# Optimization experiments

Hardware: AMD Instinct MI355X
Metric: run time of the kernel (lower is better)

## Reference

```python
import jax, jax.numpy as jnp
import numpy as np

N, S, D = 8, 448, 768
VS, DS = 50000, 256
VP, DP = 200, 128
VM, DM = 400, 128
VA, DA = 360, 128
EPS_LS = 0.1
LN_EPS = 1e-12
SQRT2 = 1.4142135623730951


def setup_inputs() -> dict:
    key = jax.random.key(0)
    ks = jax.random.split(key, 20)
    total = N * S
    # all sequence lengths == S; next-token prediction uses tokens [0, S-2] as
    # inputs (hidden_sel) and tokens [1, S-1] as targets (target_sel)
    hidden_sel = np.concatenate([i * S + np.arange(S - 1) for i in range(N)]).astype(np.int32)
    target_sel = np.concatenate([i * S + np.arange(1, S) for i in range(N)]).astype(np.int32)
    tokens_lengths = (np.arange(total) % 4).astype(np.int32)  # per-token affix counts
    affix_sel = np.nonzero(tokens_lengths[target_sel] > 0)[0].astype(np.int32)

    def p(k, shape):
        return jax.random.normal(k, shape, jnp.float32) * 0.02

    inp = {
        "tr_hidden_state": jax.random.normal(ks[0], (S, N, D), jnp.float32),
        "affixes_prob": jax.random.uniform(ks[1], (total, VA), dtype=jnp.float32),
        "stems": jax.random.randint(ks[2], (total,), 0, VS, jnp.int32),
        "pos_tags": jax.random.randint(ks[3], (total,), 0, VP, jnp.int32),
        "lm_morphs": jax.random.randint(ks[4], (total,), 0, VM, jnp.int32),
        "hidden_sel_idx": jnp.asarray(hidden_sel),
        "target_sel_idx": jnp.asarray(target_sel),
        "affix_sel_idx": jnp.asarray(affix_sel),
        # stem head
        "stem_emb": p(ks[5], (VS, DS)), "stem_W": p(ks[6], (D, DS)),
        "stem_b": jnp.zeros((DS,)), "stem_g": jnp.ones((DS,)),
        "stem_beta": jnp.zeros((DS,)), "stem_bias": jnp.zeros((VS,)),
        # pos-tag head
        "pos_emb": p(ks[7], (VP, DP)), "pos_W": p(ks[8], (D, DP)),
        "pos_b": jnp.zeros((DP,)), "pos_g": jnp.ones((DP,)),
        "pos_beta": jnp.zeros((DP,)), "pos_bias": jnp.zeros((VP,)),
        # lm-morph head
        "morph_emb": p(ks[9], (VM, DM)), "morph_W": p(ks[10], (D, DM)),
        "morph_b": jnp.zeros((DM,)), "morph_g": jnp.ones((DM,)),
        "morph_beta": jnp.zeros((DM,)), "morph_bias": jnp.zeros((VM,)),
        # affixes head
        "aff_emb": p(ks[11], (VA, DA)), "aff_W": p(ks[12], (D, DA)),
        "aff_b": jnp.zeros((DA,)), "aff_g": jnp.ones((DA,)),
        "aff_beta": jnp.zeros((DA,)), "aff_bias": jnp.zeros((VA,)),
    }
    return inp


def _gelu(x):
    return x * 0.5 * (1.0 + jax.lax.erf(x / SQRT2))


def _ln(x, g, b):
    m = x.mean(-1, keepdims=True)
    v = ((x - m) ** 2).mean(-1, keepdims=True)
    return (x - m) * jax.lax.rsqrt(v + LN_EPS) * g + b


def _head(x, W, b, g, beta, emb, bias):
    h = _ln(_gelu(x @ W + b), g, beta)  # BaseHeadTransform
    return h @ emb.T + bias             # tied decoder + bias


def _ls_nll(lprobs, tgt):
    # label_smoothed_nll_loss with reduce=True, no ignore_index
    nll = -jnp.take_along_axis(lprobs, tgt[:, None], axis=1)[:, 0]
    smooth = -lprobs.sum(-1)
    nll_m, sm_m = nll.mean(), smooth.mean()
    eps_i = EPS_LS / (lprobs.shape[-1] - 1)
    return (1.0 - EPS_LS - eps_i) * nll_m + eps_i * sm_m, nll_m


def reference(tr_hidden_state, affixes_prob, stems, pos_tags, lm_morphs,
              hidden_sel_idx, target_sel_idx, affix_sel_idx,
              stem_emb, stem_W, stem_b, stem_g, stem_beta, stem_bias,
              pos_emb, pos_W, pos_b, pos_g, pos_beta, pos_bias,
              morph_emb, morph_W, morph_b, morph_g, morph_beta, morph_bias,
              aff_emb, aff_W, aff_b, aff_g, aff_beta, aff_bias):
    flat = jnp.transpose(tr_hidden_state, (1, 0, 2)).reshape(N * S, D)
    x = flat[hidden_sel_idx]  # [T, D] ragged gather of predictor states

    stem_lp = jax.nn.log_softmax(_head(x, stem_W, stem_b, stem_g, stem_beta, stem_emb, stem_bias), axis=-1)
    stem_loss, stem_nll = _ls_nll(stem_lp, stems[target_sel_idx])

    pos_lp = jax.nn.log_softmax(_head(x, pos_W, pos_b, pos_g, pos_beta, pos_emb, pos_bias), axis=-1)
    pos_loss, pos_nll = _ls_nll(pos_lp, pos_tags[target_sel_idx])

    morph_lp = jax.nn.log_softmax(_head(x, morph_W, morph_b, morph_g, morph_beta, morph_emb, morph_bias), axis=-1)
    morph_loss, morph_nll = _ls_nll(morph_lp, lm_morphs[target_sel_idx])

    xa = x[affix_sel_idx]                                # tokens with affixes
    ta = affixes_prob[target_sel_idx][affix_sel_idx]     # [Ta, VA]
    z = _head(xa, aff_W, aff_b, aff_g, aff_beta, aff_emb, aff_bias)
    aff_loss = jnp.mean(jnp.maximum(z, 0.0) - z * ta + jnp.log1p(jnp.exp(-jnp.abs(z))))

    return jnp.stack([stem_loss, pos_loss, morph_loss, aff_loss, stem_nll, pos_nll, morph_nll])
```

## Files before the change

kernel.cpp:

```cpp
#include <hip/hip_runtime.h>
#include <cstdint>
#include <cstddef>


typedef __attribute__((ext_vector_type(8))) __bf16 bf16x8;
typedef __attribute__((ext_vector_type(4))) float f32x4;
typedef __attribute__((ext_vector_type(4))) unsigned short u16x4;
typedef __attribute__((ext_vector_type(2))) unsigned short u16x2;

namespace {
constexpr int S_LEN   = 448;
constexpr int N_SEQ   = 8;
constexpr int D_MODEL = 768;
constexpr int TPAD    = 3584;
constexpr int VS = 50000, VP = 200, VM = 400, VA = 360;
constexpr int DS_STEM = 256, DS_POS = 128, DS_MORPH = 128, DS_AFF = 128;
constexpr int VS_PAD = 50176;
constexpr int VCHUNK = 32;
constexpr int VITERS = 3136 / VCHUNK;
constexpr int PERIODS = VITERS / 2;
constexpr float PAD_E = (float)(VS_PAD - VS);
constexpr int NVB_P = 1;
constexpr int NVB_M = 2;
constexpr float LOG2E = 1.4426950408889634f;
constexpr float LN2   = 0.6931471805599453f;
constexpr int B_STEM = 448;
constexpr int B_P    = B_STEM + 112;
constexpr int B_M    = B_P + 224;
constexpr int PREP_G = TPAD * D_MODEL / 256;
constexpr int PREP_T = PREP_G + 120;
constexpr int PREP_C = PREP_T + 12753;
}

__device__ __forceinline__ unsigned short f2bf(float f) {
  unsigned int u = __float_as_uint(f);
  unsigned int r = (u + 0x7FFFu + ((u >> 16) & 1u)) >> 16;
  return (unsigned short)r;
}
__device__ __forceinline__ float bf2f(unsigned short u) {
  return __uint_as_float(((unsigned int)u) << 16);
}
__device__ __forceinline__ float fexp2(float x) {
#if __has_builtin(__builtin_amdgcn_exp2f)
  return __builtin_amdgcn_exp2f(x);
#else
  return exp2f(x);
#endif
}

__global__ __launch_bounds__(256) void prep_kernel(
    const float* __restrict__ tr, const int* __restrict__ hsel,
    const int* __restrict__ tsel, const int* __restrict__ asel,
    const int* __restrict__ stems, const int* __restrict__ postags,
    const int* __restrict__ morphs,
    unsigned short* __restrict__ x, int* __restrict__ tgtS, int* __restrict__ tgtP,
    int* __restrict__ tgtM, int* __restrict__ arow, int T, int Ta,
    const float* __restrict__ sW, const float* __restrict__ pW,
    const float* __restrict__ mW, const float* __restrict__ aW,
    unsigned short* __restrict__ wtS, unsigned short* __restrict__ wtP,
    unsigned short* __restrict__ wtM, unsigned short* __restrict__ wtA,
    const float* __restrict__ sE, const float* __restrict__ pE,
    const float* __restrict__ mE, const float* __restrict__ aE,
    const float* __restrict__ sb,
    unsigned short* __restrict__ dS, unsigned short* __restrict__ dP,
    unsigned short* __restrict__ dM, unsigned short* __restrict__ dA,
    float* __restrict__ bp) {
  __shared__ float tile[64][65];
  const int bid = blockIdx.x;
  const int tid = threadIdx.x;
  if (bid < PREP_G) {
    const size_t e = (size_t)bid * 256 + tid;
    const int t = (int)(e / D_MODEL);
    const int d = (int)(e % D_MODEL);
    float v = 0.f;
    if (t < T) {
      int idx = hsel[t];
      int n = idx / S_LEN, s = idx % S_LEN;
      v = tr[((size_t)s * N_SEQ + n) * D_MODEL + d];
    }
    x[e] = f2bf(v);
    if (e < (size_t)T) {
      int tt = tsel[e];
      tgtS[e] = stems[tt]; tgtP[e] = postags[tt]; tgtM[e] = morphs[tt];
    }
    if (e < (size_t)Ta) arow[e] = tsel[asel[e]];
  } else if (bid < PREP_T) {
    const int tt = bid - PREP_G;
    const float* W; unsigned short* Wt; int DS, kt, nt;
    if (tt < 48) { W = sW; Wt = wtS; DS = 256; kt = tt >> 2; nt = tt & 3; }
    else {
      int u = tt - 48; const int h = u / 24; u %= 24;
      kt = u >> 1; nt = u & 1; DS = 128;
      W  = (h == 0) ? pW : (h == 1) ? mW : aW;
      Wt = (h == 0) ? wtP : (h == 1) ? wtM : wtA;
    }
    const int k0 = kt * 64, n0 = nt * 64;
    const int rr = tid >> 6, cc = tid & 63;
#pragma unroll
    for (int i = 0; i < 16; ++i)
      tile[i * 4 + rr][cc] = W[(size_t)(k0 + i * 4 + rr) * DS + n0 + cc];
    __syncthreads();
#pragma unroll
    for (int i = 0; i < 16; ++i)
      Wt[(size_t)(n0 + i * 4 + rr) * D_MODEL + k0 + cc] = f2bf(tile[cc][i * 4 + rr]);
  } else {
    const size_t q = ((size_t)(bid - PREP_T) * 256 + tid) * 4;
    if (q >= 13008896) {
      const size_t local = q - 13008896;
      float4 v = make_float4(0.f, 0.f, 0.f, 0.f);
      if (local < (size_t)VS) v = *(const float4*)(sb + local);
      v.x *= LOG2E; v.y *= LOG2E; v.z *= LOG2E; v.w *= LOG2E;
      *(float4*)(bp + local) = v;
      return;
    }
    const float* src; unsigned short* dst; size_t local, real;
    float sc = 1.f;
    if (q < 12845056)      { src = sE; dst = dS; local = q;            real = 12800000; sc = LOG2E; }
    else if (q < 12877824) { src = pE; dst = dP; local = q - 12845056; real = 25600; }
    else if (q < 12943360) { src = mE; dst = dM; local = q - 12877824; real = 51200; }
    else                   { src = aE; dst = dA; local = q - 12943360; real = 46080; }
    float4 v = make_float4(0.f, 0.f, 0.f, 0.f);
    if (local < real) v = *(const float4*)(src + local);
    u16x4 o = { f2bf(v.x * sc), f2bf(v.y * sc), f2bf(v.z * sc), f2bf(v.w * sc) };
    *(u16x4*)(dst + local) = o;
  }
}

template <int NT>
__device__ __forceinline__ void head_body(
    const unsigned short* __restrict__ x, const unsigned short* __restrict__ Wt,
    const float* __restrict__ bvec, const float* __restrict__ gvec,
    const float* __restrict__ betav, unsigned short* __restrict__ hout) {
  constexpr int DS = NT * 16;
  const int lane = threadIdx.x & 63;
  const int wave = threadIdx.x >> 6;
  const int row0 = blockIdx.x * 64 + wave * 16;
  const int lrow = lane & 15;
  const int lk8  = (lane >> 4) * 8;

  f32x4 acc[NT];
#pragma unroll
  for (int nt = 0; nt < NT; ++nt) acc[nt] = f32x4{0.f, 0.f, 0.f, 0.f};

  const unsigned short* xrow = x + (size_t)(row0 + lrow) * D_MODEL + lk8;
#pragma unroll
  for (int ks = 0; ks < 24; ++ks) {
    bf16x8 a = *(const bf16x8*)(xrow + ks * 32);
#pragma unroll
    for (int nt = 0; nt < NT; ++nt) {
      bf16x8 b = *(const bf16x8*)(Wt + (size_t)(nt * 16 + lrow) * D_MODEL + ks * 32 + lk8);
      acc[nt] = __builtin_amdgcn_mfma_f32_16x16x32_bf16(a, b, acc[nt], 0, 0, 0);
    }
  }

  float bb[NT], gg[NT], be[NT];
#pragma unroll
  for (int nt = 0; nt < NT; ++nt) {
    int c = nt * 16 + lrow;
    bb[nt] = bvec[c]; gg[nt] = gvec[c]; be[nt] = betav[c];
  }
#pragma unroll
  for (int r = 0; r < 4; ++r) {
    const int row = row0 + (lane >> 4) * 4 + r;
    float vals[NT];
    float s = 0.f, s2 = 0.f;
#pragma unroll
    for (int nt = 0; nt < NT; ++nt) {
      float v = acc[nt][r] + bb[nt];
      v = 0.5f * v * (1.f + erff(v * 0.70710678118654752f));
      vals[nt] = v; s += v; s2 += v * v;
    }
    s  += __shfl_xor(s, 1);  s  += __shfl_xor(s, 2);  s  += __shfl_xor(s, 4);  s  += __shfl_xor(s, 8);
    s2 += __shfl_xor(s2, 1); s2 += __shfl_xor(s2, 2); s2 += __shfl_xor(s2, 4); s2 += __shfl_xor(s2, 8);
    const float mean = s * (1.f / DS);
    const float var  = s2 * (1.f / DS) - mean * mean;
    const float rstd = rsqrtf(var + 1e-12f);
#pragma unroll
    for (int nt = 0; nt < NT; ++nt) {
      float o = (vals[nt] - mean) * rstd * gg[nt] + be[nt];
      hout[(size_t)row * DS + nt * 16 + lrow] = f2bf(o);
    }
  }
}

__global__ __launch_bounds__(256, 2) void head_all_kernel(
    const unsigned short* __restrict__ x,
    const unsigned short* __restrict__ wtS, const float* __restrict__ sb,
    const float* __restrict__ sg, const float* __restrict__ sbe, unsigned short* __restrict__ hS,
    const unsigned short* __restrict__ wtP, const float* __restrict__ pb,
    const float* __restrict__ pg, const float* __restrict__ pbe, unsigned short* __restrict__ hP,
    const unsigned short* __restrict__ wtM, const float* __restrict__ mb,
    const float* __restrict__ mg, const float* __restrict__ mbe, unsigned short* __restrict__ hM,
    const unsigned short* __restrict__ wtA, const float* __restrict__ ab,
    const float* __restrict__ ag, const float* __restrict__ abe, unsigned short* __restrict__ hA) {
  if (blockIdx.y == 3)      head_body<16>(x, wtS, sb, sg, sbe, hS);
  else if (blockIdx.y == 0) head_body<8>(x, wtP, pb, pg, pbe, hP);
  else if (blockIdx.y == 1) head_body<8>(x, wtM, mb, mg, mbe, hM);
  else                      head_body<8>(x, wtA, ab, ag, abe, hA);
}


__device__ __forceinline__ void stem_role(
    const unsigned short* __restrict__ h, const unsigned short* __restrict__ emb,
    const float* __restrict__ bpad, float* __restrict__ psum,
    float* __restrict__ psum2, char* smem) {
  float* lbias = (float*)(smem + 49152);

  const int f    = blockIdx.x;
  const int xcd  = f & 7;
  const int m    = f >> 3;
  const int bx   = m % 14;
  const int by   = (m / 14) * 8 + xcd;
  const int tid  = threadIdx.x;
  const int lane = tid & 63;
  const int wave = tid >> 6;
  const int lrow = lane & 15;
  const int hi   = lane >> 4;
  const int lk8  = hi * 8;
  const int tok0 = bx * 256 + wave * 64;
  const int vbase0 = by * (VITERS * 16);

  for (int i = tid; i < VITERS * 16; i += 256) lbias[i] = bpad[vbase0 + i];

  bf16x8 hB[4][8];
#pragma unroll
  for (int tt = 0; tt < 4; ++tt)
#pragma unroll
    for (int ks = 0; ks < 8; ++ks)
      hB[tt][ks] = *(const bf16x8*)(h + (size_t)(tok0 + tt * 16 + lrow) * 256 + ks * 32 + lk8);

  const int d0 = tid * 16;
  const int s0 = d0 ^ (((d0 >> 9) & 7) << 4);
  const char* gsA = (const char*)emb + (size_t)vbase0 * 512 + s0;
  const char* gsB = gsA + 4096;

  auto stage_tile = [&](int buf, int tile2) {
    __builtin_amdgcn_global_load_lds(
        (const __attribute__((address_space(1))) unsigned int*)(gsA + (size_t)tile2 * 8192),
        (__attribute__((address_space(3))) unsigned int*)(smem + buf * 8192 + wave * 1024),
        16, 0, 0);
    __builtin_amdgcn_global_load_lds(
        (const __attribute__((address_space(1))) unsigned int*)(gsB + (size_t)tile2 * 8192),
        (__attribute__((address_space(3))) unsigned int*)(smem + buf * 8192 + 4096 + wave * 1024),
        16, 0, 0);
  };

  int loff[8];
#pragma unroll
  for (int ks = 0; ks < 8; ++ks)
    loff[ks] = (lrow * 512 + ks * 64 + hi * 16) ^ ((lrow & 7) << 4);

  float esum[4] = {0.f, 0.f, 0.f, 0.f};
  float ssum[4] = {0.f, 0.f, 0.f, 0.f};

  stage_tile(0, 0); stage_tile(1, 1);
  stage_tile(2, 2); stage_tile(3, 3);
  __syncthreads();

#pragma unroll 1
  for (int p = 0; p < PERIODS; ++p) {
    if (p < PERIODS - 1) asm volatile("s_waitcnt vmcnt(4)" ::: "memory");
    else                 asm volatile("s_waitcnt vmcnt(0)" ::: "memory");
    __builtin_amdgcn_s_barrier();

    const int t0 = 2 * p, t1 = 2 * p + 1;
    const int b0 = (p % 3) * 2, b1 = b0 + 1;
    const float4 bv0 = *(const float4*)(lbias + t0 * 16 + hi * 4);
    const float4 bv1 = *(const float4*)(lbias + t1 * 16 + hi * 4);

    const char* lp0 = smem + b0 * 8192;
    bf16x8 aA[8];
#pragma unroll
    for (int ks = 0; ks < 8; ++ks)
      aA[ks] = *(const bf16x8*)(lp0 + loff[ks]);

#pragma unroll
    for (int tt = 0; tt < 4; ++tt) {
      f32x4 acc = f32x4{bv0.x, bv0.y, bv0.z, bv0.w};
#pragma unroll
      for (int ks = 0; ks < 8; ++ks)
        acc = __builtin_amdgcn_mfma_f32_16x16x32_bf16(aA[ks], hB[tt][ks], acc, 0, 0, 0);
      esum[tt] += (fexp2(acc[0]) + fexp2(acc[1])) + (fexp2(acc[2]) + fexp2(acc[3]));
      ssum[tt] += (acc[0] + acc[1]) + (acc[2] + acc[3]);
    }

    const char* lp1 = smem + b1 * 8192;
    bf16x8 aB[8];
#pragma unroll
    for (int ks = 0; ks < 8; ++ks)
      aB[ks] = *(const bf16x8*)(lp1 + loff[ks]);

    if (p + 2 < PERIODS) {
      const int nb = ((p + 2) % 3) * 2;
      stage_tile(nb,     2 * (p + 2));
      stage_tile(nb + 1, 2 * (p + 2) + 1);
    }

#pragma unroll
    for (int tt = 0; tt < 4; ++tt) {
      f32x4 acc = f32x4{bv1.x, bv1.y, bv1.z, bv1.w};
#pragma unroll
      for (int ks = 0; ks < 8; ++ks)
        acc = __builtin_amdgcn_mfma_f32_16x16x32_bf16(aB[ks], hB[tt][ks], acc, 0, 0, 0);
      esum[tt] += (fexp2(acc[0]) + fexp2(acc[1])) + (fexp2(acc[2]) + fexp2(acc[3]));
      ssum[tt] += (acc[0] + acc[1]) + (acc[2] + acc[3]);
    }
  }

#pragma unroll
  for (int tt = 0; tt < 4; ++tt) {
    float e = esum[tt], s = ssum[tt];
    e += __shfl_xor(e, 16); e += __shfl_xor(e, 32);
    s += __shfl_xor(s, 16); s += __shfl_xor(s, 32);
    if (hi == 0) {
      const int tok = tok0 + tt * 16 + lrow;
      psum [(size_t)tok * VCHUNK + by] = e;
      psum2[(size_t)tok * VCHUNK + by] = s * LN2;
    }
  }
}

__device__ __forceinline__ void pm_role(
    const unsigned short* __restrict__ h, const unsigned short* __restrict__ emb,
    const float* __restrict__ bias, float* __restrict__ psum,
    float* __restrict__ psum2, int V, int NVB, int vbx, int vby, char* smem) {
  const int tid = threadIdx.x;
  const int lane = tid & 63;
  const int wave4 = tid >> 6;
  const int colbase = vby * 256 + wave4 * 64;
  const int row0 = vbx * 32;
  const int lrow = lane & 15;
  const int hi   = lane >> 4;
  const int lk8  = hi * 8;
  float (*lds_e)[32] = (float(*)[32])smem;
  float (*lds_s)[32] = (float(*)[32])(smem + 512);

  bf16x8 bfr[4][4];
  float bv[4];
  bool mk[4];
#pragma unroll
  for (int nt = 0; nt < 4; ++nt) {
    int col = colbase + nt * 16 + lrow;
#pragma unroll
    for (int ks = 0; ks < 4; ++ks)
      bfr[ks][nt] = *(const bf16x8*)(emb + (size_t)col * 128 + ks * 32 + lk8);
    mk[nt] = (col < V);
    bv[nt] = mk[nt] ? bias[col] : 0.f;
  }

  f32x4 acc[2][4];
#pragma unroll
  for (int rt = 0; rt < 2; ++rt)
#pragma unroll
    for (int nt = 0; nt < 4; ++nt) acc[rt][nt] = f32x4{0.f, 0.f, 0.f, 0.f};

  const unsigned short* hrow = h + (size_t)(row0 + lrow) * 128 + lk8;
#pragma unroll
  for (int ks = 0; ks < 4; ++ks) {
#pragma unroll
    for (int rt = 0; rt < 2; ++rt) {
      bf16x8 a = *(const bf16x8*)(hrow + (size_t)rt * 16 * 128 + ks * 32);
#pragma unroll
      for (int nt = 0; nt < 4; ++nt)
        acc[rt][nt] = __builtin_amdgcn_mfma_f32_16x16x32_bf16(a, bfr[ks][nt], acc[rt][nt], 0, 0, 0);
    }
  }

#pragma unroll
  for (int rt = 0; rt < 2; ++rt)
#pragma unroll
    for (int r = 0; r < 4; ++r) {
      float e = 0.f, s = 0.f;
#pragma unroll
      for (int nt = 0; nt < 4; ++nt) {
        float v = acc[rt][nt][r] + bv[nt];
        float ev = __expf(v);
        e += mk[nt] ? ev : 0.f;
        s += mk[nt] ? v : 0.f;
      }
      e += __shfl_xor(e, 1); e += __shfl_xor(e, 2); e += __shfl_xor(e, 4); e += __shfl_xor(e, 8);
      s += __shfl_xor(s, 1); s += __shfl_xor(s, 2); s += __shfl_xor(s, 4); s += __shfl_xor(s, 8);
      if (lrow == 0) {
        lds_e[wave4][rt * 16 + hi * 4 + r] = e;
        lds_s[wave4][rt * 16 + hi * 4 + r] = s;
      }
    }
  __syncthreads();
  if (tid < 32) {
    const int rr = tid;
    float e = lds_e[0][rr] + lds_e[1][rr] + lds_e[2][rr] + lds_e[3][rr];
    float s = lds_s[0][rr] + lds_s[1][rr] + lds_s[2][rr] + lds_s[3][rr];
    const int row = row0 + rr;
    psum [(size_t)row * NVB + vby] = e;
    psum2[(size_t)row * NVB + vby] = s;
  }
}

__device__ __forceinline__ void aff_role(
    const unsigned short* __restrict__ h, const unsigned short* __restrict__ emb,
    const float* __restrict__ bias, const int* __restrict__ asel,
    const int* __restrict__ arow, const float* __restrict__ aprob,
    float* __restrict__ partial, int Ta, int gaff, int bx, int grp, char* smem) {
  const int tid = threadIdx.x;
  const int lane = tid & 63;
  const int wave4 = tid >> 6;
  const int colbase = grp * 256 + wave4 * 64;
  const int lrow = lane & 15;
  const int lk8  = (lane >> 4) * 8;
  float* wred = (float*)smem;

  bf16x8 bfr[4][4];
  float bv[4];
  bool mk[4];
#pragma unroll
  for (int nt = 0; nt < 4; ++nt) {
    int col = colbase + nt * 16 + lrow;
#pragma unroll
    for (int ks = 0; ks < 4; ++ks)
      bfr[ks][nt] = *(const bf16x8*)(emb + (size_t)col * DS_AFF + ks * 32 + lk8);
    mk[nt] = (col < VA);
    bv[nt] = mk[nt] ? bias[col] : 0.f;
  }

  float lsum = 0.f;
  {
    const int rb = bx * 16;
    const int ia = rb + lrow;
    const int srow = (ia < Ta) ? asel[ia] : 0;
    f32x4 acc[4];
#pragma unroll
    for (int nt = 0; nt < 4; ++nt) acc[nt] = f32x4{0.f, 0.f, 0.f, 0.f};
    const unsigned short* hrow = h + (size_t)srow * DS_AFF + lk8;
#pragma unroll
    for (int ks = 0; ks < 4; ++ks) {
      bf16x8 a = *(const bf16x8*)(hrow + ks * 32);
#pragma unroll
      for (int nt = 0; nt < 4; ++nt)
        acc[nt] = __builtin_amdgcn_mfma_f32_16x16x32_bf16(a, bfr[ks][nt], acc[nt], 0, 0, 0);
    }
#pragma unroll
    for (int r = 0; r < 4; ++r) {
      const int i2 = rb + (lane >> 4) * 4 + r;
      const bool live = (i2 < Ta);
      const int trow = live ? arow[i2] : 0;
#pragma unroll
      for (int nt = 0; nt < 4; ++nt) {
        if (live && mk[nt]) {
          float z = acc[nt][r] + bv[nt];
          float ta = aprob[(size_t)trow * VA + (colbase + nt * 16 + lrow)];
          lsum += fmaxf(z, 0.f) - z * ta + log1pf(__expf(-fabsf(z)));
        }
      }
    }
  }
#pragma unroll
  for (int m = 1; m < 64; m <<= 1) lsum += __shfl_xor(lsum, m);
  if (lane == 0) wred[wave4] = lsum;
  __syncthreads();
  if (tid == 0)
    partial[grp * gaff + bx] = wred[0] + wred[1] + wred[2] + wred[3];
}

__device__ __forceinline__ void tgt_role(
    const unsigned short* __restrict__ hS, const unsigned short* __restrict__ embS,
    const float* __restrict__ bS, const int* __restrict__ tgtS_,
    const unsigned short* __restrict__ hP, const unsigned short* __restrict__ embP,
    const float* __restrict__ bP, const int* __restrict__ tgtP_,
    const unsigned short* __restrict__ hM, const unsigned short* __restrict__ embM,
    const float* __restrict__ bM, const int* __restrict__ tgtM_,
    float* __restrict__ tlog, int T, int vb) {
  const int lane = threadIdx.x & 63;
  const int wave = threadIdx.x >> 6;
  const int t = vb * 4 + wave;
  if (t >= T) return;
  const int tg = tgtS_[t], tp = tgtP_[t], tm = tgtM_[t];
  u16x4 hv = *(const u16x4*)(hS + (size_t)t * 256 + lane * 4);
  u16x4 ev = *(const u16x4*)(embS + (size_t)tg * 256 + lane * 4);
  float d0 = bf2f(hv[0]) * bf2f(ev[0]) + bf2f(hv[1]) * bf2f(ev[1]) +
             bf2f(hv[2]) * bf2f(ev[2]) + bf2f(hv[3]) * bf2f(ev[3]);
  u16x2 hp = *(const u16x2*)(hP + (size_t)t * 128 + lane * 2);
  u16x2 ep = *(const u16x2*)(embP + (size_t)tp * 128 + lane * 2);
  float d1 = bf2f(hp[0]) * bf2f(ep[0]) + bf2f(hp[1]) * bf2f(ep[1]);
  u16x2 hm = *(const u16x2*)(hM + (size_t)t * 128 + lane * 2);
  u16x2 em = *(const u16x2*)(embM + (size_t)tm * 128 + lane * 2);
  float d2 = bf2f(hm[0]) * bf2f(em[0]) + bf2f(hm[1]) * bf2f(em[1]);
#pragma unroll
  for (int m = 1; m < 64; m <<= 1) {
    d0 += __shfl_xor(d0, m); d1 += __shfl_xor(d1, m); d2 += __shfl_xor(d2, m);
  }
  if (lane == 0) {
    tlog[t]            = d0 * LN2 + bS[tg];
    tlog[TPAD + t]     = d1 + bP[tp];
    tlog[2 * TPAD + t] = d2 + bM[tm];
  }
}

__global__ __launch_bounds__(256, 2) void mega_stats_kernel(
    const unsigned short* __restrict__ hS, const unsigned short* __restrict__ embS,
    const float* __restrict__ bpadS, float* __restrict__ psS, float* __restrict__ ps2S,
    const unsigned short* __restrict__ hP, const unsigned short* __restrict__ embP,
    const float* __restrict__ p_bias, float* __restrict__ psP, float* __restrict__ ps2P,
    const unsigned short* __restrict__ hM, const unsigned short* __restrict__ embM,
    const float* __restrict__ m_bias, float* __restrict__ psM, float* __restrict__ ps2M,
    const unsigned short* __restrict__ hA, const unsigned short* __restrict__ embA,
    const float* __restrict__ a_bias, const int* __restrict__ asel,
    const int* __restrict__ arow, const float* __restrict__ aprob,
    float* __restrict__ affp,
    const float* __restrict__ s_bias, const int* __restrict__ tgtS,
    const int* __restrict__ tgtP, const int* __restrict__ tgtM,
    float* __restrict__ tlog, int T, int Ta, int gaff) {
  __shared__ alignas(16) char smem_[55424];
  const int bid = blockIdx.x;
  if (bid < B_STEM) {
    stem_role(hS, embS, bpadS, psS, ps2S, smem_);
  } else if (bid < B_P) {
    pm_role(hP, embP, p_bias, psP, ps2P, VP, NVB_P, bid - B_STEM, 0, smem_);
  } else if (bid < B_M) {
    const int b = bid - B_P;
    pm_role(hM, embM, m_bias, psM, ps2M, VM, NVB_M, b >> 1, b & 1, smem_);
  } else if (bid < B_M + 2 * gaff) {
    const int b = bid - B_M;
    aff_role(hA, embA, a_bias, asel, arow, aprob, affp, Ta, gaff, b >> 1, b & 1, smem_);
  } else {
    tgt_role(hS, embS, s_bias, tgtS, hP, embP, p_bias, tgtP,
             hM, embM, m_bias, tgtM, tlog, T, bid - B_M - 2 * gaff);
  }
}

__global__ __launch_bounds__(256) void combine2_kernel(
    const float* __restrict__ psS, const float* __restrict__ ps2S,
    const float* __restrict__ psP, const float* __restrict__ ps2P,
    const float* __restrict__ psM, const float* __restrict__ ps2M,
    const float* __restrict__ tlog,
    float* __restrict__ nll, float* __restrict__ sm, int T) {
  const int lane = threadIdx.x & 63;
  const int wave = threadIdx.x >> 6;
  const int t = blockIdx.x * 4 + wave;
  if (t >= T) return;

  float z = 0.f, s = 0.f;
  if (lane < VCHUNK) {
    z = psS[(size_t)t * VCHUNK + lane];
    s = ps2S[(size_t)t * VCHUNK + lane];
  }
#pragma unroll
  for (int m = 1; m < 64; m <<= 1) { z += __shfl_xor(z, m); s += __shfl_xor(s, m); }
  if (lane == 0) {
    z -= PAD_E;
    float lz = logf(z);
    nll[t] = lz - tlog[t];
    sm[t]  = (float)VS * lz - s;

    float zP = psP[t], sP = ps2P[t];
    float lzP = logf(zP);
    nll[TPAD + t] = lzP - tlog[TPAD + t];
    sm[TPAD + t]  = (float)VP * lzP - sP;

    float zM = psM[2 * t] + psM[2 * t + 1];
    float sM = ps2M[2 * t] + ps2M[2 * t + 1];
    float lzM = logf(zM);
    nll[2 * TPAD + t] = lzM - tlog[2 * TPAD + t];
    sm[2 * TPAD + t]  = (float)VM * lzM - sM;
  }
}

__global__ __launch_bounds__(256) void finalize_kernel(
    const float* __restrict__ nll, const float* __restrict__ sm,
    const float* __restrict__ affp, int naff, float* __restrict__ out, int T, int Ta) {
  __shared__ float red[256];
  const int tid = threadIdx.x;
  float nll_m[3], sm_m[3];
  for (int h2 = 0; h2 < 3; ++h2) {
    float a = 0.f, b = 0.f;
    for (int t = tid; t < T; t += 256) { a += nll[h2 * TPAD + t]; b += sm[h2 * TPAD + t]; }
    red[tid] = a; __syncthreads();
    for (int s = 128; s > 0; s >>= 1) { if (tid < s) red[tid] += red[tid + s]; __syncthreads(); }
    float asum = red[0]; __syncthreads();
    red[tid] = b; __syncthreads();
    for (int s = 128; s > 0; s >>= 1) { if (tid < s) red[tid] += red[tid + s]; __syncthreads(); }
    float bsm = red[0]; __syncthreads();
    nll_m[h2] = asum / (float)T;
    sm_m[h2]  = bsm / (float)T;
  }
  float av = 0.f;
  for (int i = tid; i < naff; i += 256) av += affp[i];
  red[tid] = av; __syncthreads();
  for (int s = 128; s > 0; s >>= 1) { if (tid < s) red[tid] += red[tid + s]; __syncthreads(); }
  if (tid == 0) {
    const float Vv[3] = {(float)VS, (float)VP, (float)VM};
    for (int h2 = 0; h2 < 3; ++h2) {
      float eps_i = 0.1f / (Vv[h2] - 1.f);
      out[h2] = (1.0f - 0.1f - eps_i) * nll_m[h2] + eps_i * sm_m[h2];
      out[4 + h2] = nll_m[h2];
    }
    out[3] = red[0] / ((float)Ta * (float)VA);
  }
}

extern "C" void kernel_launch(void* const* d_in, const int* in_sizes, int n_in,
                              void* d_out, int out_size, void* d_ws, size_t ws_size,
                              hipStream_t stream) {
  const float* tr      = (const float*)d_in[0];
  const float* aprob   = (const float*)d_in[1];
  const int* stems     = (const int*)d_in[2];
  const int* postags   = (const int*)d_in[3];
  const int* morphs    = (const int*)d_in[4];
  const int* hsel      = (const int*)d_in[5];
  const int* tsel      = (const int*)d_in[6];
  const int* asel      = (const int*)d_in[7];
  const float* s_emb = (const float*)d_in[8],  *s_W = (const float*)d_in[9];
  const float* s_b   = (const float*)d_in[10], *s_g = (const float*)d_in[11];
  const float* s_be  = (const float*)d_in[12], *s_bias = (const float*)d_in[13];
  const float* p_emb = (const float*)d_in[14], *p_W = (const float*)d_in[15];
  const float* p_b   = (const float*)d_in[16], *p_g = (const float*)d_in[17];
  const float* p_be  = (const float*)d_in[18], *p_bias = (const float*)d_in[19];
  const float* m_emb = (const float*)d_in[20], *m_W = (const float*)d_in[21];
  const float* m_b   = (const float*)d_in[22], *m_g = (const float*)d_in[23];
  const float* m_be  = (const float*)d_in[24], *m_bias = (const float*)d_in[25];
  const float* a_emb = (const float*)d_in[26], *a_W = (const float*)d_in[27];
  const float* a_b   = (const float*)d_in[28], *a_g = (const float*)d_in[29];
  const float* a_be  = (const float*)d_in[30], *a_bias = (const float*)d_in[31];

  const int T  = in_sizes[5];
  const int Ta = in_sizes[7];

  size_t off = 0;
  auto alloc = [&](size_t nbytes) -> char* {
    char* p = (char*)d_ws + off;
    off = (off + nbytes + 255) & ~(size_t)255;
    return p;
  };
  unsigned short* x    = (unsigned short*)alloc((size_t)TPAD * D_MODEL * 2);
  unsigned short* wtS  = (unsigned short*)alloc((size_t)DS_STEM * D_MODEL * 2);
  unsigned short* wtP  = (unsigned short*)alloc((size_t)DS_POS * D_MODEL * 2);
  unsigned short* wtM  = (unsigned short*)alloc((size_t)DS_MORPH * D_MODEL * 2);
  unsigned short* wtA  = (unsigned short*)alloc((size_t)DS_AFF * D_MODEL * 2);
  unsigned short* embS = (unsigned short*)alloc((size_t)VS_PAD * DS_STEM * 2);
  unsigned short* embP = (unsigned short*)alloc((size_t)256 * DS_POS * 2);
  unsigned short* embM = (unsigned short*)alloc((size_t)512 * DS_MORPH * 2);
  unsigned short* embA = (unsigned short*)alloc((size_t)512 * DS_AFF * 2);
  unsigned short* hS   = (unsigned short*)alloc((size_t)TPAD * DS_STEM * 2);
  unsigned short* hP   = (unsigned short*)alloc((size_t)TPAD * DS_POS * 2);
  unsigned short* hM   = (unsigned short*)alloc((size_t)TPAD * DS_MORPH * 2);
  unsigned short* hA   = (unsigned short*)alloc((size_t)TPAD * DS_AFF * 2);
  float* bpadS = (float*)alloc((size_t)VS_PAD * 4);
  float* psS   = (float*)alloc((size_t)TPAD * VCHUNK * 4);
  float* ps2S  = (float*)alloc((size_t)TPAD * VCHUNK * 4);
  float* psP   = (float*)alloc((size_t)TPAD * NVB_P * 4);
  float* ps2P  = (float*)alloc((size_t)TPAD * NVB_P * 4);
  float* psM   = (float*)alloc((size_t)TPAD * NVB_M * 4);
  float* ps2M  = (float*)alloc((size_t)TPAD * NVB_M * 4);
  float* tlog  = (float*)alloc((size_t)3 * TPAD * 4);
  int*   tgtS  = (int*)alloc((size_t)TPAD * 4);
  int*   tgtP  = (int*)alloc((size_t)TPAD * 4);
  int*   tgtM  = (int*)alloc((size_t)TPAD * 4);
  int*   arow  = (int*)alloc((size_t)TPAD * 4);
  float* nllb  = (float*)alloc((size_t)3 * TPAD * 4);
  float* smb   = (float*)alloc((size_t)3 * TPAD * 4);
  float* affp  = (float*)alloc(2048);
  (void)ws_size; (void)n_in; (void)out_size;

  const int gaff = (Ta + 15) / 16;
  const int tgtb = (T + 3) / 4;

  prep_kernel<<<PREP_C, 256, 0, stream>>>(
      tr, hsel, tsel, asel, stems, postags, morphs, x, tgtS, tgtP, tgtM, arow, T, Ta,
      s_W, p_W, m_W, a_W, wtS, wtP, wtM, wtA,
      s_emb, p_emb, m_emb, a_emb, s_bias, embS, embP, embM, embA, bpadS);
  head_all_kernel<<<dim3(TPAD / 64, 4), 256, 0, stream>>>(
      x, wtS, s_b, s_g, s_be, hS, wtP, p_b, p_g, p_be, hP,
      wtM, m_b, m_g, m_be, hM, wtA, a_b, a_g, a_be, hA);
  mega_stats_kernel<<<B_M + 2 * gaff + tgtb, 256, 0, stream>>>(
      hS, embS, bpadS, psS, ps2S,
      hP, embP, p_bias, psP, ps2P,
      hM, embM, m_bias, psM, ps2M,
      hA, embA, a_bias, asel, arow, aprob, affp,
      s_bias, tgtS, tgtP, tgtM, tlog, T, Ta, gaff);
  combine2_kernel<<<(T + 3) / 4, 256, 0, stream>>>(psS, ps2S, psP, ps2P, psM, ps2M, tlog, nllb, smb, T);
  finalize_kernel<<<1, 256, 0, stream>>>(nllb, smb, affp, gaff * 2, (float*)d_out, T, Ta);
}
```

Before: 221.2 us.

## Vectorize gather, change LDS swizzle, and coarsen small-head and target blocks

The prep gather now loads float4 and writes four bf16 per thread, using a quarter as many blocks. The stem-role LDS swizzle changes from an XOR pattern to a rotating chunk offset, to alter how bank conflicts fall. In the stats kernel, the pos/morph, affix and target-logit roles each process several tiles or tokens per block, cutting the block count and per-block setup. A trailing barrier is added to pm_role so smem can be reused across consecutive calls. Blocks now do more serial work, which lowers parallelism for these small roles.

```diff
diff --git a/kernel.cpp b/kernel.cpp
--- a/kernel.cpp
+++ b/kernel.cpp
@@ -25,9 +25,9 @@
 constexpr float LOG2E = 1.4426950408889634f;
 constexpr float LN2   = 0.6931471805599453f;
 constexpr int B_STEM = 448;
-constexpr int B_P    = B_STEM + 112;
-constexpr int B_M    = B_P + 224;
-constexpr int PREP_G = TPAD * D_MODEL / 256;
+constexpr int B_P    = B_STEM + 56;
+constexpr int B_M    = B_P + 112;
+constexpr int PREP_G = TPAD * D_MODEL / 1024;
 constexpr int PREP_T = PREP_G + 120;
 constexpr int PREP_C = PREP_T + 12753;
 }
@@ -69,21 +69,23 @@
   const int bid = blockIdx.x;
   const int tid = threadIdx.x;
   if (bid < PREP_G) {
-    const size_t e = (size_t)bid * 256 + tid;
+    const int e4 = bid * 256 + tid;
+    const size_t e = (size_t)e4 * 4;
     const int t = (int)(e / D_MODEL);
     const int d = (int)(e % D_MODEL);
-    float v = 0.f;
+    float4 v = make_float4(0.f, 0.f, 0.f, 0.f);
     if (t < T) {
       int idx = hsel[t];
       int n = idx / S_LEN, s = idx % S_LEN;
-      v = tr[((size_t)s * N_SEQ + n) * D_MODEL + d];
-    }
-    x[e] = f2bf(v);
-    if (e < (size_t)T) {
-      int tt = tsel[e];
-      tgtS[e] = stems[tt]; tgtP[e] = postags[tt]; tgtM[e] = morphs[tt];
-    }
-    if (e < (size_t)Ta) arow[e] = tsel[asel[e]];
+      v = *(const float4*)(tr + ((size_t)s * N_SEQ + n) * D_MODEL + d);
+    }
+    u16x4 o = { f2bf(v.x), f2bf(v.y), f2bf(v.z), f2bf(v.w) };
+    *(u16x4*)(x + e) = o;
+    if (e4 < T) {
+      int tt = tsel[e4];
+      tgtS[e4] = stems[tt]; tgtP[e4] = postags[tt]; tgtM[e4] = morphs[tt];
+    }
+    if (e4 < Ta) arow[e4] = tsel[asel[e4]];
   } else if (bid < PREP_T) {
     const int tt = bid - PREP_G;
     const float* W; unsigned short* Wt; int DS, kt, nt;
@@ -230,7 +232,9 @@
       hB[tt][ks] = *(const bf16x8*)(h + (size_t)(tok0 + tt * 16 + lrow) * 256 + ks * 32 + lk8);
 
   const int d0 = tid * 16;
-  const int s0 = d0 ^ (((d0 >> 9) & 7) << 4);
+  const int srow0 = d0 >> 9;
+  const int sch  = (((d0 >> 4) & 31) - 4 * srow0) & 31;
+  const int s0   = (srow0 << 9) + (sch << 4);
   const char* gsA = (const char*)emb + (size_t)vbase0 * 512 + s0;
   const char* gsB = gsA + 4096;
 
@@ -248,7 +252,7 @@
   int loff[8];
 #pragma unroll
   for (int ks = 0; ks < 8; ++ks)
-    loff[ks] = (lrow * 512 + ks * 64 + hi * 16) ^ ((lrow & 7) << 4);
+    loff[ks] = (lrow << 9) + ((((ks << 2) + hi + (lrow << 2)) & 31) << 4);
 
   float esum[4] = {0.f, 0.f, 0.f, 0.f};
   float ssum[4] = {0.f, 0.f, 0.f, 0.f};
@@ -394,13 +398,14 @@
     psum [(size_t)row * NVB + vby] = e;
     psum2[(size_t)row * NVB + vby] = s;
   }
+  __syncthreads();
 }
 
 __device__ __forceinline__ void aff_role(
     const unsigned short* __restrict__ h, const unsigned short* __restrict__ emb,
     const float* __restrict__ bias, const int* __restrict__ asel,
     const int* __restrict__ arow, const float* __restrict__ aprob,
-    float* __restrict__ partial, int Ta, int gaff, int bx, int grp, char* smem) {
+    float* __restrict__ partial, int Ta, int gaff64, int bx, int grp, char* smem) {
   const int tid = threadIdx.x;
   const int lane = tid & 63;
   const int wave4 = tid >> 6;
@@ -423,8 +428,8 @@
   }
 
   float lsum = 0.f;
-  {
-    const int rb = bx * 16;
+  for (int it = 0; it < 4; ++it) {
+    const int rb = bx * 64 + it * 16;
     const int ia = rb + lrow;
     const int srow = (ia < Ta) ? asel[ia] : 0;
     f32x4 acc[4];
@@ -458,7 +463,7 @@
   if (lane == 0) wred[wave4] = lsum;
   __syncthreads();
   if (tid == 0)
-    partial[grp * gaff + bx] = wred[0] + wred[1] + wred[2] + wred[3];
+    partial[grp * gaff64 + bx] = wred[0] + wred[1] + wred[2] + wred[3];
 }
 
 __device__ __forceinline__ void tgt_role(
@@ -471,27 +476,30 @@
     float* __restrict__ tlog, int T, int vb) {
   const int lane = threadIdx.x & 63;
   const int wave = threadIdx.x >> 6;
-  const int t = vb * 4 + wave;
-  if (t >= T) return;
-  const int tg = tgtS_[t], tp = tgtP_[t], tm = tgtM_[t];
-  u16x4 hv = *(const u16x4*)(hS + (size_t)t * 256 + lane * 4);
-  u16x4 ev = *(const u16x4*)(embS + (size_t)tg * 256 + lane * 4);
-  float d0 = bf2f(hv[0]) * bf2f(ev[0]) + bf2f(hv[1]) * bf2f(ev[1]) +
-             bf2f(hv[2]) * bf2f(ev[2]) + bf2f(hv[3]) * bf2f(ev[3]);
-  u16x2 hp = *(const u16x2*)(hP + (size_t)t * 128 + lane * 2);
-  u16x2 ep = *(const u16x2*)(embP + (size_t)tp * 128 + lane * 2);
-  float d1 = bf2f(hp[0]) * bf2f(ep[0]) + bf2f(hp[1]) * bf2f(ep[1]);
-  u16x2 hm = *(const u16x2*)(hM + (size_t)t * 128 + lane * 2);
-  u16x2 em = *(const u16x2*)(embM + (size_t)tm * 128 + lane * 2);
-  float d2 = bf2f(hm[0]) * bf2f(em[0]) + bf2f(hm[1]) * bf2f(em[1]);
-#pragma unroll
-  for (int m = 1; m < 64; m <<= 1) {
-    d0 += __shfl_xor(d0, m); d1 += __shfl_xor(d1, m); d2 += __shfl_xor(d2, m);
-  }
-  if (lane == 0) {
-    tlog[t]            = d0 * LN2 + bS[tg];
-    tlog[TPAD + t]     = d1 + bP[tp];
-    tlog[2 * TPAD + t] = d2 + bM[tm];
+#pragma unroll 1
+  for (int i = 0; i < 4; ++i) {
+    const int t = vb * 16 + wave * 4 + i;
+    if (t >= T) return;
+    const int tg = tgtS_[t], tp = tgtP_[t], tm = tgtM_[t];
+    u16x4 hv = *(const u16x4*)(hS + (size_t)t * 256 + lane * 4);
+    u16x4 ev = *(const u16x4*)(embS + (size_t)tg * 256 + lane * 4);
+    float d0 = bf2f(hv[0]) * bf2f(ev[0]) + bf2f(hv[1]) * bf2f(ev[1]) +
+               bf2f(hv[2]) * bf2f(ev[2]) + bf2f(hv[3]) * bf2f(ev[3]);
+    u16x2 hp = *(const u16x2*)(hP + (size_t)t * 128 + lane * 2);
+    u16x2 ep = *(const u16x2*)(embP + (size_t)tp * 128 + lane * 2);
+    float d1 = bf2f(hp[0]) * bf2f(ep[0]) + bf2f(hp[1]) * bf2f(ep[1]);
+    u16x2 hm = *(const u16x2*)(hM + (size_t)t * 128 + lane * 2);
+    u16x2 em = *(const u16x2*)(embM + (size_t)tm * 128 + lane * 2);
+    float d2 = bf2f(hm[0]) * bf2f(em[0]) + bf2f(hm[1]) * bf2f(em[1]);
+#pragma unroll
+    for (int m = 1; m < 64; m <<= 1) {
+      d0 += __shfl_xor(d0, m); d1 += __shfl_xor(d1, m); d2 += __shfl_xor(d2, m);
+    }
+    if (lane == 0) {
+      tlog[t]            = d0 * LN2 + bS[tg];
+      tlog[TPAD + t]     = d1 + bP[tp];
+      tlog[2 * TPAD + t] = d2 + bM[tm];
+    }
   }
 }
 
@@ -508,22 +516,25 @@
     float* __restrict__ affp,
     const float* __restrict__ s_bias, const int* __restrict__ tgtS,
     const int* __restrict__ tgtP, const int* __restrict__ tgtM,
-    float* __restrict__ tlog, int T, int Ta, int gaff) {
+    float* __restrict__ tlog, int T, int Ta, int gaff64) {
   __shared__ alignas(16) char smem_[55424];
   const int bid = blockIdx.x;
   if (bid < B_STEM) {
     stem_role(hS, embS, bpadS, psS, ps2S, smem_);
   } else if (bid < B_P) {
-    pm_role(hP, embP, p_bias, psP, ps2P, VP, NVB_P, bid - B_STEM, 0, smem_);
+    const int b = bid - B_STEM;
+    pm_role(hP, embP, p_bias, psP, ps2P, VP, NVB_P, b * 2, 0, smem_);
+    pm_role(hP, embP, p_bias, psP, ps2P, VP, NVB_P, b * 2 + 1, 0, smem_);
   } else if (bid < B_M) {
     const int b = bid - B_P;
-    pm_role(hM, embM, m_bias, psM, ps2M, VM, NVB_M, b >> 1, b & 1, smem_);
-  } else if (bid < B_M + 2 * gaff) {
+    pm_role(hM, embM, m_bias, psM, ps2M, VM, NVB_M, b, 0, smem_);
+    pm_role(hM, embM, m_bias, psM, ps2M, VM, NVB_M, b, 1, smem_);
+  } else if (bid < B_M + 2 * gaff64) {
     const int b = bid - B_M;
-    aff_role(hA, embA, a_bias, asel, arow, aprob, affp, Ta, gaff, b >> 1, b & 1, smem_);
+    aff_role(hA, embA, a_bias, asel, arow, aprob, affp, Ta, gaff64, b >> 1, b & 1, smem_);
   } else {
     tgt_role(hS, embS, s_bias, tgtS, hP, embP, p_bias, tgtP,
-             hM, embM, m_bias, tgtM, tlog, T, bid - B_M - 2 * gaff);
+             hM, embM, m_bias, tgtM, tlog, T, bid - B_M - 2 * gaff64);
   }
 }
 
@@ -660,8 +671,8 @@
   float* affp  = (float*)alloc(2048);
   (void)ws_size; (void)n_in; (void)out_size;
 
-  const int gaff = (Ta + 15) / 16;
-  const int tgtb = (T + 3) / 4;
+  const int gaff64 = (Ta + 63) / 64;
+  const int tgtb   = (T + 15) / 16;
 
   prep_kernel<<<PREP_C, 256, 0, stream>>>(
       tr, hsel, tsel, asel, stems, postags, morphs, x, tgtS, tgtP, tgtM, arow, T, Ta,
@@ -670,12 +681,12 @@
   head_all_kernel<<<dim3(TPAD / 64, 4), 256, 0, stream>>>(
       x, wtS, s_b, s_g, s_be, hS, wtP, p_b, p_g, p_be, hP,
       wtM, m_b, m_g, m_be, hM, wtA, a_b, a_g, a_be, hA);
-  mega_stats_kernel<<<B_M + 2 * gaff + tgtb, 256, 0, stream>>>(
+  mega_stats_kernel<<<B_M + 2 * gaff64 + tgtb, 256, 0, stream>>>(
       hS, embS, bpadS, psS, ps2S,
       hP, embP, p_bias, psP, ps2P,
       hM, embM, m_bias, psM, ps2M,
       hA, embA, a_bias, asel, arow, aprob, affp,
-      s_bias, tgtS, tgtP, tgtM, tlog, T, Ta, gaff);
+      s_bias, tgtS, tgtP, tgtM, tlog, T, Ta, gaff64);
   combine2_kernel<<<(T + 3) / 4, 256, 0, stream>>>(psS, ps2S, psP, ps2P, psM, ps2M, tlog, nllb, smb, T);
-  finalize_kernel<<<1, 256, 0, stream>>>(nllb, smb, affp, gaff * 2, (float*)d_out, T, Ta);
-}
+  finalize_kernel<<<1, 256, 0, stream>>>(nllb, smb, affp, gaff64 * 2, (float*)d_out, T, Ta);
+}
```

Result: slower. 228.3 us, median of 2 (+3.2%).
